# Kernel tuning notes

Measured on AMD Instinct MI355X. Metric: run time of the kernel, lower is better.

## Reference

```python
import jax, jax.numpy as jnp
import numpy as np

SQ, B, NP, HN = 2048, 2, 16, 64  # [seq, batch, heads, head_dim]

def setup_inputs() -> dict:
    key = jax.random.key(0)
    kq, kk, kv = jax.random.split(key, 3)
    return {
        "query": jax.random.normal(kq, (SQ, B, NP, HN), dtype=jnp.float32),
        "key":   jax.random.normal(kk, (SQ, B, NP, HN), dtype=jnp.float32),
        "value": jax.random.normal(kv, (SQ, B, NP, HN), dtype=jnp.float32),
    }

def reference(query, key, value):
    sq, b, nheads, hn = query.shape
    # NOTE: original module computes norm_factor=sqrt(hn) but never applies it;
    # scores are UNscaled QK^T, replicated faithfully here.
    scores = jnp.einsum('sbnh,tbnh->bnst', query, key)          # [b, np, sq, sk]
    probs = jax.nn.softmax(scores, axis=-1)                      # mask=None -> plain softmax
    # dropout is deterministic (train=False default) -> identity
    context = jnp.einsum('bnst,tbnh->sbnh', probs, value)        # [sq, b, np, hn]
    return context.reshape(sq, b, nheads * hn).astype(jnp.float32)
```

## Files before the change

### kernel.cpp

```cpp
#include <hip/hip_runtime.h>
#include <math.h>
#include <stdint.h>

#define SQ 2048
#define NBH 32
#define HN 64
#define BQ 128
#define BK2 128
#define NP2 (SQ/BK2)
#define TOK 2048
#define HSTRIDE (SQ*HN)

typedef _Float16 half2v __attribute__((ext_vector_type(2)));
typedef _Float16 half4v __attribute__((ext_vector_type(4)));
typedef _Float16 half8v __attribute__((ext_vector_type(8)));
typedef float f32x16 __attribute__((ext_vector_type(16)));

__device__ __forceinline__ void async16(const void* g, void* l) {
  __builtin_amdgcn_global_load_lds(
      (const __attribute__((address_space(1))) void*)g,
      (__attribute__((address_space(3))) void*)l, 16, 0, 0);
}

__device__ __forceinline__ float fexp2(float x) {
#if __has_builtin(__builtin_amdgcn_exp2f)
  return __builtin_amdgcn_exp2f(x);
#else
  return exp2f(x);
#endif
}

__device__ __forceinline__ float xmax32(float x) {
#if __has_builtin(__builtin_amdgcn_permlane32_swap)
  auto r = __builtin_amdgcn_permlane32_swap(__float_as_int(x), __float_as_int(x),
                                            false, false);
  return fmaxf(__int_as_float(r[0]), __int_as_float(r[1]));
#else
  return fmaxf(x, __shfl_xor(x, 32, 64));
#endif
}
__device__ __forceinline__ float xadd32(float x) {
#if __has_builtin(__builtin_amdgcn_permlane32_swap)
  auto r = __builtin_amdgcn_permlane32_swap(__float_as_int(x), __float_as_int(x),
                                            false, false);
  return __int_as_float(r[0]) + __int_as_float(r[1]);
#else
  return x + __shfl_xor(x, 32, 64);
#endif
}

__global__ __launch_bounds__(256) void prep_kv(const float* __restrict__ K,
                                               const float* __restrict__ V,
                                               _Float16* __restrict__ Kh,
                                               _Float16* __restrict__ Vt) {
  __shared__ _Float16 vs[HN * 64];
  const int t = threadIdx.x;
  const int pflat = blockIdx.y * 32 + blockIdx.x;
  const int head = (pflat & 7) + 8 * (pflat >> 8);
  const int ck = (pflat >> 3) & 31;
  {
    const int key = ck * 64 + (t >> 2);
    const int c0 = (t & 3) * 2;
    const float* src = K + (size_t)key * TOK + head * HN + c0 * 8;
    float4 a = *(const float4*)src;
    float4 b = *(const float4*)(src + 4);
    float4 c = *(const float4*)(src + 8);
    float4 d = *(const float4*)(src + 12);
    half8v h0, h1;
    h0[0]=(_Float16)a.x; h0[1]=(_Float16)a.y; h0[2]=(_Float16)a.z; h0[3]=(_Float16)a.w;
    h0[4]=(_Float16)b.x; h0[5]=(_Float16)b.y; h0[6]=(_Float16)b.z; h0[7]=(_Float16)b.w;
    h1[0]=(_Float16)c.x; h1[1]=(_Float16)c.y; h1[2]=(_Float16)c.z; h1[3]=(_Float16)c.w;
    h1[4]=(_Float16)d.x; h1[5]=(_Float16)d.y; h1[6]=(_Float16)d.z; h1[7]=(_Float16)d.w;
    _Float16* row = Kh + (size_t)head * HSTRIDE + (size_t)key * 64;
    *(half8v*)&row[((c0    ) ^ (key & 7)) * 8] = h0;
    *(half8v*)&row[((c0 + 1) ^ (key & 7)) * 8] = h1;
  }
  {
    const int kt = ck * 64;
    const int kl = (t >> 3) * 2;
    const int db = (t & 7) * 8;
    const float* src = V + (size_t)(kt + kl) * TOK + head * HN + db;
    float4 a0 = *(const float4*)src;
    float4 a1 = *(const float4*)(src + 4);
    float4 b0 = *(const float4*)(src + TOK);
    float4 b1 = *(const float4*)(src + TOK + 4);
    const float av[8] = {a0.x,a0.y,a0.z,a0.w,a1.x,a1.y,a1.z,a1.w};
    const float bv[8] = {b0.x,b0.y,b0.z,b0.w,b1.x,b1.y,b1.z,b1.w};
    const int u = kl >> 2;
    #pragma unroll
    for (int j = 0; j < 8; ++j) {
      const int dim = db + j;
      const int pos = u ^ (dim & 15);
      half2v h; h[0] = (_Float16)av[j]; h[1] = (_Float16)bv[j];
      *(half2v*)&vs[dim * 64 + pos * 4 + (kl & 3)] = h;
    }
    __syncthreads();
    const int dim = t >> 2;
    const int q = (t & 3) ^ (dim & 3);
    const _Float16* srow = &vs[dim * 64 + q * 16];
    _Float16* drow = Vt + (size_t)head * HSTRIDE + (size_t)dim * SQ + kt + q * 16;
    *(half8v*)&drow[0] = *(const half8v*)&srow[0];
    *(half8v*)&drow[8] = *(const half8v*)&srow[8];
  }
}

__global__ __launch_bounds__(512, 4)
void fattn_mfma(const float* __restrict__ Q, const _Float16* __restrict__ Kh,
                const _Float16* __restrict__ Vt, float* __restrict__ O) {
  __shared__ __align__(16) _Float16 smem[4 * 8192];
  _Float16* kbf = smem;
  _Float16* vtf = smem + 16384;

  const int t = threadIdx.x;
  const int lane = t & 63;
  const int w = t >> 6;
  const int qw = w & 3;
  const int g = w >> 2;
  const int h2 = lane >> 5;
  const int l31 = lane & 31;
  const int pflat = blockIdx.y * 16 + blockIdx.x;
  const int head = (pflat & 7) + 8 * (pflat >> 7);
  const int qc = (pflat >> 3) & 15;
  const int q0 = qc * BQ + qw * 32;
  const _Float16* Kp = Kh + (size_t)head * HSTRIDE;
  const _Float16* Vp = Vt + (size_t)head * HSTRIDE;
  const int tb = g * 4096;

  half8v qf[4];
  {
    const float* qp = Q + (size_t)(q0 + l31) * TOK + head * HN + 8 * h2;
    const float s = 1.44269504088896f;
    #pragma unroll
    for (int ks = 0; ks < 4; ++ks) {
      float4 a = *(const float4*)(qp + 16 * ks);
      float4 b = *(const float4*)(qp + 16 * ks + 4);
      half8v f;
      f[0] = (_Float16)(s*a.x); f[1] = (_Float16)(s*a.y); f[2] = (_Float16)(s*a.z); f[3] = (_Float16)(s*a.w);
      f[4] = (_Float16)(s*b.x); f[5] = (_Float16)(s*b.y); f[6] = (_Float16)(s*b.z); f[7] = (_Float16)(s*b.w);
      qf[ks] = f;
    }
  }

  f32x16 acc0, acc1;
  #pragma unroll
  for (int r = 0; r < 16; ++r) { acc0[r] = 0.f; acc1[r] = 0.f; }
  float m_i = -INFINITY, l_i = 0.f;

  auto stage = [&](int p) {
    const int buf = p & 1;
    const size_t kt = (size_t)p * BK2;
    #pragma unroll
    for (int i = 0; i < 2; ++i) {
      const int off = w * 512 + i * 4096;
      async16(Kp + kt * 64 + off + lane * 8, kbf + buf * 8192 + off);
    }
    #pragma unroll
    for (int tl = 0; tl < 2; ++tl) {
      const int off = w * 512;
      const int eo = off + lane * 8;
      const int dim = eo >> 6, inner = eo & 63;
      async16(Vp + (size_t)dim * SQ + kt + tl * 64 + inner,
              vtf + buf * 8192 + tl * 4096 + off);
    }
  };

  auto phase = [&](int p, int cur) {
    __syncthreads();
    if (p + 1 < NP2) stage(p + 1);
    const _Float16* kb = kbf + cur * 8192 + tb;
    const _Float16* vb = vtf + cur * 8192 + tb;

    f32x16 c0, c1;
    #pragma unroll
    for (int r = 0; r < 16; ++r) { c0[r] = 0.f; c1[r] = 0.f; }
    __builtin_amdgcn_s_setprio(1);
    #pragma unroll
    for (int ks = 0; ks < 4; ++ks) {
      const int pos = ((h2 + 2 * ks) ^ (l31 & 7)) * 8;
      half8v a0v = *(const half8v*)&kb[l31 * 64 + pos];
      half8v a1v = *(const half8v*)&kb[(l31 + 32) * 64 + pos];
      c0 = __builtin_amdgcn_mfma_f32_32x32x16_f16(a0v, qf[ks], c0, 0, 0, 0);
      c1 = __builtin_amdgcn_mfma_f32_32x32x16_f16(a1v, qf[ks], c1, 0, 0, 0);
    }
    __builtin_amdgcn_s_setprio(0);

    float tv[16];
    #pragma unroll
    for (int r = 0; r < 16; ++r) tv[r] = fmaxf(c0[r], c1[r]);
    float ma = fmaxf(fmaxf(tv[0], tv[1]), tv[2]);
    float mb = fmaxf(fmaxf(tv[3], tv[4]), tv[5]);
    float mc = fmaxf(fmaxf(tv[6], tv[7]), tv[8]);
    float md = fmaxf(fmaxf(tv[9], tv[10]), tv[11]);
    ma = fmaxf(fmaxf(ma, tv[12]), tv[13]);
    mb = fmaxf(fmaxf(mb, tv[14]), tv[15]);
    float mx = xmax32(fmaxf(fmaxf(ma, mb), fmaxf(mc, md)));
    if (!__all(mx <= m_i + 8.f)) {
      const float mnew = fmaxf(m_i, mx);
      const float alpha = fexp2(m_i - mnew);
      l_i *= alpha;
      m_i = mnew;
      #pragma unroll
      for (int r = 0; r < 16; ++r) { acc0[r] *= alpha; acc1[r] *= alpha; }
    }
    float rs0 = 0.f, rs1 = 0.f;
    #pragma unroll
    for (int r = 0; r < 16; ++r) {
      float p0 = fexp2(c0[r] - m_i);
      float p1 = fexp2(c1[r] - m_i);
      c0[r] = p0; c1[r] = p1;
      rs0 += p0; rs1 += p1;
    }
    l_i += xadd32(rs0 + rs1);

    __builtin_amdgcn_s_setprio(1);
    #pragma unroll
    for (int ks = 0; ks < 4; ++ks) {
      const int rb = 8 * (ks & 1);
      const f32x16& s = (ks < 2) ? c0 : c1;
      union { half8v v8; half2v v2[4]; } pu;
      #pragma unroll
      for (int tt = 0; tt < 4; ++tt) {
        auto pk = __builtin_amdgcn_cvt_pkrtz(s[rb + 2 * tt], s[rb + 2 * tt + 1]);
        pu.v2[tt] = *(half2v*)&pk;
      }
      #pragma unroll
      for (int mbd = 0; mbd < 2; ++mbd) {
        const int dim = l31 + 32 * mbd;
        const int sw = dim & 15;
        union { half8v v8; half4v v4[2]; } au;
        au.v4[0] = *(const half4v*)&vb[dim * 64 + ((4 * ks + h2)     ^ sw) * 4];
        au.v4[1] = *(const half4v*)&vb[dim * 64 + ((4 * ks + 2 + h2) ^ sw) * 4];
        if (mbd == 0)
          acc0 = __builtin_amdgcn_mfma_f32_32x32x16_f16(au.v8, pu.v8, acc0, 0, 0, 0);
        else
          acc1 = __builtin_amdgcn_mfma_f32_32x32x16_f16(au.v8, pu.v8, acc1, 0, 0, 0);
      }
    }
    __builtin_amdgcn_s_setprio(0);
  };

  stage(0);
  #pragma unroll 1
  for (int p = 0; p < NP2; p += 2) {
    phase(p, 0);
    phase(p + 1, 1);
  }

  __syncthreads();
  float* fb = (float*)smem;
  const int slot = qw * 64 + lane;
  if (g == 1) {
    #pragma unroll
    for (int r = 0; r < 16; ++r) {
      fb[slot * 33 + r]      = acc0[r];
      fb[slot * 33 + 16 + r] = acc1[r];
    }
    fb[8448 + slot] = m_i;
    fb[8704 + slot] = l_i;
  }
  __syncthreads();
  if (g == 0) {
    const float m2 = fb[8448 + slot];
    const float l2 = fb[8704 + slot];
    const float ms = fmaxf(m_i, m2);
    const float a0 = fexp2(m_i - ms);
    const float a1 = fexp2(m2 - ms);
    const float invl = 1.f / (l_i * a0 + l2 * a1);
    float* orow = O + (size_t)(q0 + l31) * TOK + head * HN;
    #pragma unroll
    for (int r = 0; r < 16; ++r) {
      const int d = (r & 3) + 8 * (r >> 2) + 4 * h2;
      orow[d]      = (acc0[r] * a0 + fb[slot * 33 + r]      * a1) * invl;
      orow[d + 32] = (acc1[r] * a0 + fb[slot * 33 + 16 + r] * a1) * invl;
    }
  }
}

extern "C" void kernel_launch(void* const* d_in, const int* in_sizes, int n_in,
                              void* d_out, int out_size, void* d_ws, size_t ws_size,
                              hipStream_t stream) {
  const float* Q = (const float*)d_in[0];
  const float* K = (const float*)d_in[1];
  const float* V = (const float*)d_in[2];
  float* O = (float*)d_out;
  _Float16* Kh = (_Float16*)d_ws;
  _Float16* Vh = Kh + (size_t)NBH * HSTRIDE;
  prep_kv<<<dim3(SQ / 64, NBH), 256, 0, stream>>>(K, V, Kh, Vh);
  fattn_mfma<<<dim3(SQ / BQ, NBH), 512, 0, stream>>>(Q, Kh, Vh, O);
}
```

Baseline: 141.4 us.

## Triple-buffer K/V tiles in LDS with explicit vmcnt waits

Replaces the two-stage double buffer with a three-buffer ring, prefetching two tiles ahead and waiting on partial vmcnt instead of a full barrier per phase. Shared memory grows to 96KB dynamic, set via a function attribute, and launch bounds are relaxed to 2 waves-groups per CU. It is meant to hide global-to-LDS latency better, but the extra LDS reduces resident blocks per CU and may lower occupancy.

```diff
diff --git a/kernel.cpp b/kernel.cpp
--- a/kernel.cpp
+++ b/kernel.cpp
@@ -104,12 +104,12 @@
   }
 }
 
-__global__ __launch_bounds__(512, 4)
+__global__ __launch_bounds__(512, 2)
 void fattn_mfma(const float* __restrict__ Q, const _Float16* __restrict__ Kh,
                 const _Float16* __restrict__ Vt, float* __restrict__ O) {
-  __shared__ __align__(16) _Float16 smem[4 * 8192];
+  extern __shared__ __align__(16) _Float16 smem[];
   _Float16* kbf = smem;
-  _Float16* vtf = smem + 16384;
+  _Float16* vtf = smem + 24576;
 
   const int t = threadIdx.x;
   const int lane = t & 63;
@@ -146,8 +146,7 @@
   for (int r = 0; r < 16; ++r) { acc0[r] = 0.f; acc1[r] = 0.f; }
   float m_i = -INFINITY, l_i = 0.f;
 
-  auto stage = [&](int p) {
-    const int buf = p & 1;
+  auto stage = [&](int p, int buf) {
     const size_t kt = (size_t)p * BK2;
     #pragma unroll
     for (int i = 0; i < 2; ++i) {
@@ -164,9 +163,19 @@
     }
   };
 
-  auto phase = [&](int p, int cur) {
-    __syncthreads();
-    if (p + 1 < NP2) stage(p + 1);
+  stage(0, 0);
+  stage(1, 1);
+  int cur = 0, nxt = 2;
+  #pragma unroll 1
+  for (int p = 0; p < NP2; ++p) {
+    if (p + 1 < NP2) {
+      asm volatile("s_waitcnt vmcnt(4)" ::: "memory");
+    } else {
+      asm volatile("s_waitcnt vmcnt(0)" ::: "memory");
+    }
+    __builtin_amdgcn_s_barrier();
+    __builtin_amdgcn_sched_barrier(0);
+    if (p + 2 < NP2) stage(p + 2, nxt);
     const _Float16* kb = kbf + cur * 8192 + tb;
     const _Float16* vb = vtf + cur * 8192 + tb;
 
@@ -237,13 +246,9 @@
       }
     }
     __builtin_amdgcn_s_setprio(0);
-  };
-
-  stage(0);
-  #pragma unroll 1
-  for (int p = 0; p < NP2; p += 2) {
-    phase(p, 0);
-    phase(p + 1, 1);
+
+    cur = (cur == 2) ? 0 : cur + 1;
+    nxt = (nxt == 2) ? 0 : nxt + 1;
   }
 
   __syncthreads();
@@ -285,6 +290,12 @@
   float* O = (float*)d_out;
   _Float16* Kh = (_Float16*)d_ws;
   _Float16* Vh = Kh + (size_t)NBH * HSTRIDE;
-  prep_kv<<<dim3(SQ / 64, NBH), 256, 0, stream>>>(K, V, Kh, Vh);
-  fattn_mfma<<<dim3(SQ / BQ, NBH), 512, 0, stream>>>(Q, Kh, Vh, O);
-}
+  static bool attr_done = false;
+  if (!attr_done) {
+    hipFuncSetAttribute(reinterpret_cast<const void*>(fattn_mfma),
+                        hipFuncAttributeMaxDynamicSharedMemorySize, 98304);
+    attr_done = true;
+  }
+  prep_kv<<<dim3(32, 32), 256, 0, stream>>>(K, V, Kh, Vh);
+  fattn_mfma<<<dim3(SQ / BQ, NBH), 512, 98304, stream>>>(Q, Kh, Vh, O);
+}
```

New measurement: 150.6 us. 1.07x slower.
